# Performance work log

Measured on AMD Instinct MI355X. Metric: run time of the kernel, lower is better.

Reference implementation:

```python
import jax, jax.numpy as jnp
import numpy as np

N = 50000
E = 800000
IN_DIM = 256
HID = 64
HEADS0 = 4
HEADS1 = 1
NUM_CLASSES = 64
NEG_SLOPE = 0.2


def setup_inputs() -> dict:
    key = jax.random.key(0)
    ks = jax.random.split(key, 9)
    x = jax.random.normal(ks[0], (N, IN_DIM), dtype=jnp.float32)
    src0 = jax.random.randint(ks[1], (E,), 0, N, dtype=jnp.int32)
    dst0 = jax.random.randint(ks[2], (E,), 0, N, dtype=jnp.int32)
    src1 = jax.random.randint(ks[3], (E,), 0, N, dtype=jnp.int32)
    dst1 = jax.random.randint(ks[4], (E,), 0, N, dtype=jnp.int32)
    # layer 0: fc (share_weights -> single W), attn vector per head
    W0 = jax.random.normal(ks[5], (IN_DIM, HEADS0 * HID), dtype=jnp.float32) * (1.0 / np.sqrt(IN_DIM))
    attn0 = jax.random.normal(ks[6], (HEADS0, HID), dtype=jnp.float32) * (1.0 / np.sqrt(HID))
    # layer 1 (final): input dim = HID*HEADS0, out = NUM_CLASSES per head
    W1 = jax.random.normal(ks[7], (HID * HEADS0, HEADS1 * NUM_CLASSES), dtype=jnp.float32) * (1.0 / np.sqrt(HID * HEADS0))
    attn1 = jax.random.normal(ks[8], (HEADS1, NUM_CLASSES), dtype=jnp.float32) * (1.0 / np.sqrt(NUM_CLASSES))
    return {"x": x, "W0": W0, "attn0": attn0, "W1": W1, "attn1": attn1,
            "src0": src0, "dst0": dst0, "src1": src1, "dst1": dst1}


def gatv2_conv(h, W, attn, src, dst, n_nodes):
    """DGL GATv2Conv with share_weights=True, bias=False, residual=False.
    h: [N, Fin], W: [Fin, H*D], attn: [H, D]. Returns [N, H, D]."""
    H, D = attn.shape
    feat = (h @ W).reshape(n_nodes, H, D)          # [N, H, D]
    fs = feat[src]                                  # [E, H, D] gather src
    fd = feat[dst]                                  # [E, H, D] gather dst
    # e_ij = a^T LeakyReLU(W h_i + W h_j)
    e = jnp.einsum('ehd,hd->eh', jax.nn.leaky_relu(fs + fd, NEG_SLOPE), attn)  # [E, H]
    # edge softmax over incoming edges of each dst node (stable)
    m = jax.ops.segment_max(e, dst, num_segments=n_nodes)    # [N, H]
    ex = jnp.exp(e - m[dst])                                  # [E, H]
    s = jax.ops.segment_sum(ex, dst, num_segments=n_nodes)   # [N, H]
    alpha = ex / s[dst]                                       # [E, H]
    out = jax.ops.segment_sum(alpha[:, :, None] * fs, dst, num_segments=n_nodes)  # [N, H, D]
    return out


def reference(x, W0, attn0, W1, attn1, src0, dst0, src1, dst1):
    h = gatv2_conv(x, W0, attn0, src0, dst0, N)      # [N, 4, 64]
    h = jax.nn.elu(h)                                 # layer activation
    h = h.reshape(N, HEADS0 * HID)                    # flatten(1)
    h = gatv2_conv(h, W1, attn1, src1, dst1, N)       # [N, 1, 64], no activation
    logits = h.mean(axis=1)                           # mean over heads -> [N, 64]
    return logits
```

## Files before the change

kernel.cpp:

```cpp
#include <hip/hip_runtime.h>

#define N_NODES 50000
#define E_EDGES 800000
#define NEG_SLOPE 0.2f
#define NSL 8
#define SLN (NSL * N_NODES)
#define NB1 196
#define ROWS_PAD 50048
#define GB0 782
#define EB 3125
#define NBE0 12500
#define CAP 16

typedef __attribute__((ext_vector_type(8))) _Float16 f16x8;
typedef __attribute__((ext_vector_type(4))) float f32x4;
typedef __attribute__((ext_vector_type(4))) _Float16 half4v;
typedef __attribute__((ext_vector_type(2))) _Float16 half2v;

union H4 { half4v h4; half2v h2[2]; unsigned u[2]; };

__device__ __forceinline__ void gload_lds16(const void* g, void* l) {
    __builtin_amdgcn_global_load_lds((__attribute__((address_space(1))) void*)g,
                                     (__attribute__((address_space(3))) void*)l, 16, 0, 0);
}

#define LOG2E 1.4426950408889634f

__device__ __forceinline__ float score4(half4v g, half4v fd, const H4& A6, const H4& A4) {
    H4 Z; Z.h4 = g + fd;
    H4 B; B.u[0] = Z.u[0] & 0x7FFF7FFFu; B.u[1] = Z.u[1] & 0x7FFF7FFFu;
    float p = __builtin_amdgcn_fdot2(Z.h2[0], A6.h2[0], 0.0f, false);
    p = __builtin_amdgcn_fdot2(Z.h2[1], A6.h2[1], p, false);
    p = __builtin_amdgcn_fdot2(B.h2[0], A4.h2[0], p, false);
    p = __builtin_amdgcn_fdot2(B.h2[1], A4.h2[1], p, false);
    return p;
}

__device__ __forceinline__ void wimg_one(const float* W, _Float16* img, int Nc, int i) {
    int col = i >> 5, chunk = i & 31;
    int CT = Nc >> 4;
    int kb = chunk >> 2, ct = col >> 4;
    int li = (col & 15) + (chunk & 3) * 16;
    size_t base = ((size_t)kb * CT + ct) * 512 + li * 8;
    half4v v0, v1;
#pragma unroll
    for (int e = 0; e < 4; ++e) v0[e] = (_Float16)W[(size_t)(chunk * 8 + e) * Nc + col];
#pragma unroll
    for (int e = 0; e < 4; ++e) v1[e] = (_Float16)W[(size_t)(chunk * 8 + 4 + e) * Nc + col];
    *(half4v*)&img[base]     = v0;
    *(half4v*)&img[base + 4] = v1;
}


__global__ void k_init(const float* __restrict__ W0, const float* __restrict__ W1,
                       _Float16* __restrict__ img0, _Float16* __restrict__ img1,
                       int* __restrict__ cnt_s) {
    int gtid = blockIdx.x * 256 + threadIdx.x;
    if (gtid < 2 * SLN / 4) ((int4*)cnt_s)[gtid] = make_int4(0, 0, 0, 0);
    if (gtid < 256 * 32) wimg_one(W0, img0, 256, gtid);
    else if (gtid < 256 * 32 + 64 * 32) wimg_one(W1, img1, 64, gtid - 256 * 32);
}


__global__ __launch_bounds__(256, 4) void k_gemm0_scat(const float* __restrict__ X,
                                                       const _Float16* __restrict__ Bimg,
                                                       _Float16* __restrict__ C, int M,
                                                       const int* __restrict__ src0,
                                                       const int* __restrict__ dst0,
                                                       const int* __restrict__ src1,
                                                       const int* __restrict__ dst1,
                                                       int* __restrict__ cnt_s,
                                                       unsigned short* __restrict__ buck) {
    constexpr int CT = 16;
    __shared__ __align__(16) _Float16 AsF[4 * 512];
    __shared__ __align__(16) _Float16 Bs[CT * 512];

    if (blockIdx.x >= GB0) {
        int hb = blockIdx.x - GB0;
        int layer = (hb >= EB) ? 1 : 0;
        int bi = hb - layer * EB;
        int slice = bi & (NSL - 1);
        int i = bi * 256 + threadIdx.x;
        int s = (layer == 0) ? src0[i] : src1[i];
        int d = (layer == 0) ? dst0[i] : dst1[i];
        size_t sn = (size_t)layer * SLN + slice * N_NODES + d;
        int pos = atomicAdd(&cnt_s[sn], 1);
        if (pos < CAP) buck[(sn << 4) + pos] = (unsigned short)s;
        return;
    }

    const int t = threadIdx.x;
    const int w = t >> 6;
    const int lane = t & 63;
    const int r16 = lane & 15;
    const int kg = lane >> 4;
    const int bm = blockIdx.x * 64;
    const int arow = bm + w * 16 + r16;
    const bool rv = (arow < M);
    const float* xsrc = X + (size_t)arow * 256 + kg * 8;

    f32x4 acc[CT];
#pragma unroll
    for (int j = 0; j < CT; ++j) acc[j] = (f32x4){0.f, 0.f, 0.f, 0.f};

    for (int kb = 0; kb < 8; ++kb) {
        float4 v0 = make_float4(0.f, 0.f, 0.f, 0.f);
        float4 v1 = make_float4(0.f, 0.f, 0.f, 0.f);
        if (rv) {
            v0 = *(const float4*)(xsrc + kb * 32);
            v1 = *(const float4*)(xsrc + kb * 32 + 4);
        }
        f16x8 af;
        af[0] = (_Float16)v0.x; af[1] = (_Float16)v0.y;
        af[2] = (_Float16)v0.z; af[3] = (_Float16)v0.w;
        af[4] = (_Float16)v1.x; af[5] = (_Float16)v1.y;
        af[6] = (_Float16)v1.z; af[7] = (_Float16)v1.w;
        *(f16x8*)&AsF[t * 8] = af;
#pragma unroll
        for (int p = 0; p < CT / 4; ++p)
            gload_lds16(Bimg + kb * CT * 512 + p * 2048 + t * 8, &Bs[p * 2048 + w * 512]);
        __syncthreads();

        const f16x8 aF = *(const f16x8*)&AsF[t * 8];
#pragma unroll
        for (int ct = 0; ct < CT; ++ct) {
            const f16x8 b = *(const f16x8*)&Bs[ct * 512 + lane * 8];
            acc[ct] = __builtin_amdgcn_mfma_f32_16x16x32_f16(aF, b, acc[ct], 0, 0, 0);
        }
        __syncthreads();
    }

#pragma unroll
    for (int r = 0; r < 4; ++r) {
        int row = bm + w * 16 + kg * 4 + r;
        if (row < M) {
#pragma unroll
            for (int ct = 0; ct < CT; ++ct)
                C[(size_t)row * 256 + ct * 16 + r16] = (_Float16)acc[ct][r];
        }
    }
}


__global__ void k_scanA(const int* __restrict__ cnt_s, int* __restrict__ rowptr,
                        int* __restrict__ bsum1) {
    const int layer = blockIdx.y;
    __shared__ int lds[256];
    int t = threadIdx.x;
    int i = blockIdx.x * 256 + t;
    int v = 0;
    if (i < N_NODES) {
        const int* d = cnt_s + layer * SLN + i;
#pragma unroll
        for (int s = 0; s < NSL; ++s) v += d[s * N_NODES];
    }
    lds[t] = v;
    __syncthreads();
    for (int off = 1; off < 256; off <<= 1) {
        int u = (t >= off) ? lds[t - off] : 0;
        __syncthreads();
        lds[t] += u;
        __syncthreads();
    }
    if (i < N_NODES) rowptr[layer * (N_NODES + 1) + i + 1] = lds[t];
    if (t == 255) bsum1[layer * 256 + blockIdx.x] = lds[255];
}

__global__ void k_scanB(const int* __restrict__ bsum1, int* __restrict__ boff1) {
    const int layer = blockIdx.x;
    __shared__ int lds[256];
    int t = threadIdx.x;
    int v = (t < NB1) ? bsum1[layer * 256 + t] : 0;
    lds[t] = v;
    __syncthreads();
    for (int off = 1; off < 256; off <<= 1) {
        int u = (t >= off) ? lds[t - off] : 0;
        __syncthreads();
        lds[t] += u;
        __syncthreads();
    }
    if (t < NB1) boff1[layer * 256 + t] = lds[t] - v;
}

__global__ void k_scanC(const int* __restrict__ boff1, int* __restrict__ rowptr) {
    const int layer = blockIdx.y;
    int i = blockIdx.x * 256 + threadIdx.x;
    if (i >= N_NODES) return;
    int* rp = rowptr + layer * (N_NODES + 1);
    rp[i + 1] += boff1[layer * 256 + (i >> 8)];
    if (i == 0) rp[0] = 0;
}


__device__ __forceinline__ void regroup_node(const int* __restrict__ cnt_s,
                                             const int* __restrict__ rowptr,
                                             const unsigned short* __restrict__ buck,
                                             int* __restrict__ csr,
                                             int layer, int node, int lane, int sh) {
    const int base = layer * SLN;
    int dg = 0;
    if (lane < NSL) dg = cnt_s[base + lane * N_NODES + node];
    int excl = 0, total = 0;
#pragma unroll
    for (int ss = 0; ss < NSL; ++ss) {
        int v = __shfl(dg, ss);
        if (ss < (lane & 7)) excl += v;
        total += v;
    }
    const int base_out = rowptr[layer * (N_NODES + 1) + node];
    int* cdst = csr + (size_t)layer * E_EDGES;
    for (int r0 = 0; r0 < total; r0 += 64) {
        int r = r0 + lane;
        bool active = (r < total);
        int rr = active ? r : 0;
        int s = 0;
#pragma unroll
        for (int ss = 1; ss < NSL; ++ss) {
            int e = __shfl(excl, ss);
            if (rr >= e) s = ss;
        }
        int eS = __shfl(excl, s);
        if (active) {
            int val = buck[(((size_t)base + s * N_NODES + node) << 4) + (r - eS)];
            cdst[base_out + r] = val << sh;
        }
    }
}


__global__ __launch_bounds__(256) void k_regroup0(const int* __restrict__ cnt_s,
                                                  const int* __restrict__ rowptr,
                                                  const unsigned short* __restrict__ buck,
                                                  int* __restrict__ csr) {
    const int lane = threadIdx.x & 63;
    const int node = blockIdx.x * 4 + (threadIdx.x >> 6);
    if (node >= N_NODES) return;
    regroup_node(cnt_s, rowptr, buck, csr, 0, node, lane, 9);
}


__global__ __launch_bounds__(256) void gat_edge0(const _Float16* __restrict__ feat,
                                                 const float* __restrict__ attn,
                                                 const int* __restrict__ rowptr,
                                                 const int* __restrict__ csr,
                                                 _Float16* __restrict__ h0img) {
    const int lane = threadIdx.x & 63;
    const int node = blockIdx.x * 4 + (threadIdx.x >> 6);
    if (node >= N_NODES) return;
    const int dbase = ((lane >> 4) << 6) + (lane & 15) * 4;
    const float4 a = *(const float4*)&attn[dbase];
    H4 A6, A4;
    A6.h4 = (half4v){(_Float16)(0.6f * LOG2E * a.x), (_Float16)(0.6f * LOG2E * a.y),
                     (_Float16)(0.6f * LOG2E * a.z), (_Float16)(0.6f * LOG2E * a.w)};
    A4.h4 = (half4v){(_Float16)(0.4f * LOG2E * a.x), (_Float16)(0.4f * LOG2E * a.y),
                     (_Float16)(0.4f * LOG2E * a.z), (_Float16)(0.4f * LOG2E * a.w)};
    const char* fbase = (const char*)feat + dbase * 2;
    const half4v fd4 = *(const half4v*)(fbase + ((size_t)node << 9));
    const int beg = rowptr[node], end = rowptr[node + 1];
    float s = 0.f, ax = 0.f, ay = 0.f, az = 0.f, aw = 0.f;
    int j = beg;
    for (; j + 7 < end; j += 8) {
        half4v g[8];
        float p[8];
#pragma unroll
        for (int i = 0; i < 8; ++i) g[i] = *(const half4v*)(fbase + csr[j + i]);
#pragma unroll
        for (int i = 0; i < 8; ++i) p[i] = score4(g[i], fd4, A6, A4);
#pragma unroll
        for (int r = 1; r <= 8; r <<= 1)
#pragma unroll
            for (int i = 0; i < 8; ++i) p[i] += __shfl_xor(p[i], r);
        float e[8];
#pragma unroll
        for (int i = 0; i < 8; ++i) e[i] = __builtin_amdgcn_exp2f(p[i]);
#pragma unroll
        for (int i = 0; i < 8; ++i) {
            s  += e[i];
            ax += e[i] * (float)g[i][0];
            ay += e[i] * (float)g[i][1];
            az += e[i] * (float)g[i][2];
            aw += e[i] * (float)g[i][3];
        }
    }
    if (j + 3 < end) {
        half4v g[4];
        float p[4];
#pragma unroll
        for (int i = 0; i < 4; ++i) g[i] = *(const half4v*)(fbase + csr[j + i]);
#pragma unroll
        for (int i = 0; i < 4; ++i) p[i] = score4(g[i], fd4, A6, A4);
#pragma unroll
        for (int r = 1; r <= 8; r <<= 1)
#pragma unroll
            for (int i = 0; i < 4; ++i) p[i] += __shfl_xor(p[i], r);
#pragma unroll
        for (int i = 0; i < 4; ++i) {
            float e = __builtin_amdgcn_exp2f(p[i]);
            s  += e;
            ax += e * (float)g[i][0];
            ay += e * (float)g[i][1];
            az += e * (float)g[i][2];
            aw += e * (float)g[i][3];
        }
        j += 4;
    }
    for (; j < end; ++j) {
        half4v g0 = *(const half4v*)(fbase + csr[j]);
        float p0 = score4(g0, fd4, A6, A4);
        p0 += __shfl_xor(p0, 1);
        p0 += __shfl_xor(p0, 2);
        p0 += __shfl_xor(p0, 4);
        p0 += __shfl_xor(p0, 8);
        float e0 = __builtin_amdgcn_exp2f(p0);
        s  += e0;
        ax += e0 * (float)g0[0];
        ay += e0 * (float)g0[1];
        az += e0 * (float)g0[2];
        aw += e0 * (float)g0[3];
    }
    float inv = (end > beg) ? (1.0f / s) : 0.f;
    half4v o;
    float v;
    v = ax * inv; o[0] = (_Float16)((v > 0.f) ? v : (__expf(v) - 1.f));
    v = ay * inv; o[1] = (_Float16)((v > 0.f) ? v : (__expf(v) - 1.f));
    v = az * inv; o[2] = (_Float16)((v > 0.f) ? v : (__expf(v) - 1.f));
    v = aw * inv; o[3] = (_Float16)((v > 0.f) ? v : (__expf(v) - 1.f));
    const int rtg = node >> 4;
    const int kb = dbase >> 5;
    const int li = (node & 15) + ((dbase >> 3) & 3) * 16;
    const size_t idx = ((size_t)rtg * 8 + kb) * 512 + li * 8 + (dbase & 7);
    *(half4v*)&h0img[idx] = o;
}


__global__ __launch_bounds__(256, 4) void k_gemm1_regroup1(const _Float16* __restrict__ Aimg,
                                                           const _Float16* __restrict__ Bimg,
                                                           _Float16* __restrict__ C, int M,
                                                           const int* __restrict__ cnt_s,
                                                           const int* __restrict__ rowptr,
                                                           const unsigned short* __restrict__ buck,
                                                           int* __restrict__ csr) {
    constexpr int CT = 4;
    __shared__ __align__(16) _Float16 AsF[4 * 512];
    __shared__ __align__(16) _Float16 Bs[CT * 512];

    if (blockIdx.x >= GB0) {
        const int lane = threadIdx.x & 63;
        const int node = (blockIdx.x - GB0) * 4 + (threadIdx.x >> 6);
        if (node >= N_NODES) return;
        regroup_node(cnt_s, rowptr, buck, csr, 1, node, lane, 7);
        return;
    }

    const int t = threadIdx.x;
    const int w = t >> 6;
    const int lane = t & 63;
    const int r16 = lane & 15;
    const int kg = lane >> 4;
    const int bm = blockIdx.x * 64;

    f32x4 acc[CT];
#pragma unroll
    for (int j = 0; j < CT; ++j) acc[j] = (f32x4){0.f, 0.f, 0.f, 0.f};

    const size_t abase = ((size_t)(blockIdx.x * 4 + w)) * 8 * 512;

    for (int kb = 0; kb < 8; ++kb) {
        gload_lds16(Aimg + abase + kb * 512 + lane * 8, &AsF[w * 512]);
        gload_lds16(Bimg + kb * CT * 512 + t * 8, &Bs[w * 512]);
        __syncthreads();

        const f16x8 aF = *(const f16x8*)&AsF[w * 512 + lane * 8];
#pragma unroll
        for (int ct = 0; ct < CT; ++ct) {
            const f16x8 b = *(const f16x8*)&Bs[ct * 512 + lane * 8];
            acc[ct] = __builtin_amdgcn_mfma_f32_16x16x32_f16(aF, b, acc[ct], 0, 0, 0);
        }
        __syncthreads();
    }

#pragma unroll
    for (int r = 0; r < 4; ++r) {
        int row = bm + w * 16 + kg * 4 + r;
        if (row < M) {
#pragma unroll
            for (int ct = 0; ct < CT; ++ct)
                C[(size_t)row * 64 + ct * 16 + r16] = (_Float16)acc[ct][r];
        }
    }
}


__global__ __launch_bounds__(256) void gat_edge1(const _Float16* __restrict__ feat,
                                                 const float* __restrict__ attn,
                                                 const int* __restrict__ rowptr,
                                                 const int* __restrict__ csr,
                                                 float* __restrict__ out) {
    const int lane = threadIdx.x & 63;
    const int node = blockIdx.x * 4 + (threadIdx.x >> 6);
    if (node >= N_NODES) return;
    const int g = lane >> 4;
    const int d0 = (lane & 15) * 4;
    const float4 a = *(const float4*)&attn[d0];
    H4 A6, A4;
    A6.h4 = (half4v){(_Float16)(0.6f * LOG2E * a.x), (_Float16)(0.6f * LOG2E * a.y),
                     (_Float16)(0.6f * LOG2E * a.z), (_Float16)(0.6f * LOG2E * a.w)};
    A4.h4 = (half4v){(_Float16)(0.4f * LOG2E * a.x), (_Float16)(0.4f * LOG2E * a.y),
                     (_Float16)(0.4f * LOG2E * a.z), (_Float16)(0.4f * LOG2E * a.w)};
    const char* fbase = (const char*)feat + d0 * 2;
    const half4v fd4 = *(const half4v*)(fbase + ((size_t)node << 7));
    const int beg = rowptr[node], end = rowptr[node + 1];
    float s = 0.f, ax = 0.f, ay = 0.f, az = 0.f, aw = 0.f;
    int j = beg + g;
    for (; j + 4 < end; j += 8) {
        half4v g0 = *(const half4v*)(fbase + csr[j]);
        half4v g1 = *(const half4v*)(fbase + csr[j + 4]);
        float p0 = score4(g0, fd4, A6, A4);
        float p1 = score4(g1, fd4, A6, A4);
        p0 += __shfl_xor(p0, 1); p1 += __shfl_xor(p1, 1);
        p0 += __shfl_xor(p0, 2); p1 += __shfl_xor(p1, 2);
        p0 += __shfl_xor(p0, 4); p1 += __shfl_xor(p1, 4);
        p0 += __shfl_xor(p0, 8); p1 += __shfl_xor(p1, 8);
        float e0 = __builtin_amdgcn_exp2f(p0);
        float e1 = __builtin_amdgcn_exp2f(p1);
        s  += e0 + e1;
        ax += e0 * (float)g0[0] + e1 * (float)g1[0];
        ay += e0 * (float)g0[1] + e1 * (float)g1[1];
        az += e0 * (float)g0[2] + e1 * (float)g1[2];
        aw += e0 * (float)g0[3] + e1 * (float)g1[3];
    }
    if (j < end) {
        half4v g0 = *(const half4v*)(fbase + csr[j]);
        float p = score4(g0, fd4, A6, A4);
        p += __shfl_xor(p, 1);
        p += __shfl_xor(p, 2);
        p += __shfl_xor(p, 4);
        p += __shfl_xor(p, 8);
        float e = __builtin_amdgcn_exp2f(p);
        s  += e;
        ax += e * (float)g0[0];
        ay += e * (float)g0[1];
        az += e * (float)g0[2];
        aw += e * (float)g0[3];
    }
#pragma unroll
    for (int off = 16; off <= 32; off <<= 1) {
        s  += __shfl_xor(s, off);
        ax += __shfl_xor(ax, off);
        ay += __shfl_xor(ay, off);
        az += __shfl_xor(az, off);
        aw += __shfl_xor(aw, off);
    }
    if (g == 0) {
        float inv = (end > beg) ? (1.0f / s) : 0.f;
        float4 o = make_float4(ax * inv, ay * inv, az * inv, aw * inv);
        *(float4*)&out[(size_t)node * 64 + d0] = o;
    }
}


extern "C" void kernel_launch(void* const* d_in, const int* in_sizes, int n_in,
                              void* d_out, int out_size, void* d_ws, size_t ws_size,
                              hipStream_t stream) {
    const float* x     = (const float*)d_in[0];
    const float* W0    = (const float*)d_in[1];
    const float* attn0 = (const float*)d_in[2];
    const float* W1    = (const float*)d_in[3];
    const float* attn1 = (const float*)d_in[4];
    const int*   src0  = (const int*)d_in[5];
    const int*   dst0  = (const int*)d_in[6];
    const int*   src1  = (const int*)d_in[7];
    const int*   dst1  = (const int*)d_in[8];
    float* out = (float*)d_out;

    _Float16* h0img  = (_Float16*)d_ws;
    _Float16* feat0h = h0img + (size_t)ROWS_PAD * 256;
    _Float16* W0img  = feat0h + (size_t)N_NODES * 256;
    _Float16* W1img  = W0img + 256 * 256;
    _Float16* feat1h = feat0h;

    int* cnt_s  = (int*)(W1img + 64 * 256);
    int* rowptr = cnt_s + 2 * SLN;
    int* bsum1  = rowptr + 2 * (N_NODES + 1);
    int* boff1  = bsum1 + 512;
    int* csr    = boff1 + 512;
    unsigned short* buck = (unsigned short*)(csr + 2 * E_EDGES);

    k_init<<<GB0, 256, 0, stream>>>(W0, W1, W0img, W1img, cnt_s);

    k_gemm0_scat<<<GB0 + 2 * EB, 256, 0, stream>>>(x, W0img, feat0h, N_NODES,
                                                   src0, dst0, src1, dst1, cnt_s, buck);

    k_scanA<<<dim3(NB1, 2), 256, 0, stream>>>(cnt_s, rowptr, bsum1);
    k_scanB<<<2,            256, 0, stream>>>(bsum1, boff1);
    k_scanC<<<dim3(NB1, 2), 256, 0, stream>>>(boff1, rowptr);

    k_regroup0<<<NBE0, 256, 0, stream>>>(cnt_s, rowptr, buck, csr);

    gat_edge0<<<NBE0, 256, 0, stream>>>(feat0h, attn0, rowptr, csr, h0img);

    k_gemm1_regroup1<<<GB0 + NBE0, 256, 0, stream>>>(h0img, W1img, feat1h, N_NODES,
                                                     cnt_s, rowptr, buck, csr);

    gat_edge1<<<NBE0, 256, 0, stream>>>(feat1h, attn1, rowptr + (N_NODES + 1),
                                        csr + E_EDGES, out);
}
```

Measured before the change: 239.7 us.

## Drop CSR build; read edge buckets directly in edge-softmax kernels

Removes the three prefix-scan kernels and both regroup passes that turned per-slice buckets into a CSR array. The edge kernels now compute per-node slice prefixes with warp shuffles and gather neighbor offsets straight from the bucket array. Count zeroing moves to a memset, and the weight-image build is merged into the scatter kernel, which now runs separately from GEMM0. This cuts several launches and a full CSR write and read, but loses the overlap of the scatter with GEMM0. It also caps in-degree per slice at CAP, so edges beyond 16 per slice are silently dropped.

```diff
diff --git a/kernel.cpp b/kernel.cpp
--- a/kernel.cpp
+++ b/kernel.cpp
@@ -5,12 +5,12 @@
 #define NEG_SLOPE 0.2f
 #define NSL 8
 #define SLN (NSL * N_NODES)
-#define NB1 196
 #define ROWS_PAD 50048
 #define GB0 782
 #define EB 3125
 #define NBE0 12500
 #define CAP 16
+#define WIB 40
 
 typedef __attribute__((ext_vector_type(8))) _Float16 f16x8;
 typedef __attribute__((ext_vector_type(4))) float f32x4;
@@ -52,33 +52,14 @@
 }
 
 
-__global__ void k_init(const float* __restrict__ W0, const float* __restrict__ W1,
-                       _Float16* __restrict__ img0, _Float16* __restrict__ img1,
-                       int* __restrict__ cnt_s) {
-    int gtid = blockIdx.x * 256 + threadIdx.x;
-    if (gtid < 2 * SLN / 4) ((int4*)cnt_s)[gtid] = make_int4(0, 0, 0, 0);
-    if (gtid < 256 * 32) wimg_one(W0, img0, 256, gtid);
-    else if (gtid < 256 * 32 + 64 * 32) wimg_one(W1, img1, 64, gtid - 256 * 32);
-}
-
-
-__global__ __launch_bounds__(256, 4) void k_gemm0_scat(const float* __restrict__ X,
-                                                       const _Float16* __restrict__ Bimg,
-                                                       _Float16* __restrict__ C, int M,
-                                                       const int* __restrict__ src0,
-                                                       const int* __restrict__ dst0,
-                                                       const int* __restrict__ src1,
-                                                       const int* __restrict__ dst1,
-                                                       int* __restrict__ cnt_s,
-                                                       unsigned short* __restrict__ buck) {
-    constexpr int CT = 16;
-    __shared__ __align__(16) _Float16 AsF[4 * 512];
-    __shared__ __align__(16) _Float16 Bs[CT * 512];
-
-    if (blockIdx.x >= GB0) {
-        int hb = blockIdx.x - GB0;
-        int layer = (hb >= EB) ? 1 : 0;
-        int bi = hb - layer * EB;
+__global__ void k_scat_wimg(const int* __restrict__ src0, const int* __restrict__ dst0,
+                            const int* __restrict__ src1, const int* __restrict__ dst1,
+                            int* __restrict__ cnt_s, unsigned short* __restrict__ buck,
+                            const float* __restrict__ W0, const float* __restrict__ W1,
+                            _Float16* __restrict__ img0, _Float16* __restrict__ img1) {
+    if (blockIdx.x < 2 * EB) {
+        int layer = (blockIdx.x >= EB) ? 1 : 0;
+        int bi = blockIdx.x - layer * EB;
         int slice = bi & (NSL - 1);
         int i = bi * 256 + threadIdx.x;
         int s = (layer == 0) ? src0[i] : src1[i];
@@ -88,6 +69,18 @@
         if (pos < CAP) buck[(sn << 4) + pos] = (unsigned short)s;
         return;
     }
+    int gtid = (blockIdx.x - 2 * EB) * 256 + threadIdx.x;
+    if (gtid < 256 * 32) wimg_one(W0, img0, 256, gtid);
+    else if (gtid < 256 * 32 + 64 * 32) wimg_one(W1, img1, 64, gtid - 256 * 32);
+}
+
+
+__global__ __launch_bounds__(256, 4) void mfma_gemm0(const float* __restrict__ X,
+                                                     const _Float16* __restrict__ Bimg,
+                                                     _Float16* __restrict__ C, int M) {
+    constexpr int CT = 16;
+    __shared__ __align__(16) _Float16 AsF[4 * 512];
+    __shared__ __align__(16) _Float16 Bs[CT * 512];
 
     const int t = threadIdx.x;
     const int w = t >> 6;
@@ -142,107 +135,45 @@
 }
 
 
-__global__ void k_scanA(const int* __restrict__ cnt_s, int* __restrict__ rowptr,
-                        int* __restrict__ bsum1) {
-    const int layer = blockIdx.y;
-    __shared__ int lds[256];
-    int t = threadIdx.x;
-    int i = blockIdx.x * 256 + t;
-    int v = 0;
-    if (i < N_NODES) {
-        const int* d = cnt_s + layer * SLN + i;
-#pragma unroll
-        for (int s = 0; s < NSL; ++s) v += d[s * N_NODES];
-    }
-    lds[t] = v;
-    __syncthreads();
-    for (int off = 1; off < 256; off <<= 1) {
-        int u = (t >= off) ? lds[t - off] : 0;
-        __syncthreads();
-        lds[t] += u;
-        __syncthreads();
-    }
-    if (i < N_NODES) rowptr[layer * (N_NODES + 1) + i + 1] = lds[t];
-    if (t == 255) bsum1[layer * 256 + blockIdx.x] = lds[255];
-}
-
-__global__ void k_scanB(const int* __restrict__ bsum1, int* __restrict__ boff1) {
-    const int layer = blockIdx.x;
-    __shared__ int lds[256];
-    int t = threadIdx.x;
-    int v = (t < NB1) ? bsum1[layer * 256 + t] : 0;
-    lds[t] = v;
-    __syncthreads();
-    for (int off = 1; off < 256; off <<= 1) {
-        int u = (t >= off) ? lds[t - off] : 0;
-        __syncthreads();
-        lds[t] += u;
-        __syncthreads();
-    }
-    if (t < NB1) boff1[layer * 256 + t] = lds[t] - v;
-}
-
-__global__ void k_scanC(const int* __restrict__ boff1, int* __restrict__ rowptr) {
-    const int layer = blockIdx.y;
-    int i = blockIdx.x * 256 + threadIdx.x;
-    if (i >= N_NODES) return;
-    int* rp = rowptr + layer * (N_NODES + 1);
-    rp[i + 1] += boff1[layer * 256 + (i >> 8)];
-    if (i == 0) rp[0] = 0;
-}
-
-
-__device__ __forceinline__ void regroup_node(const int* __restrict__ cnt_s,
-                                             const int* __restrict__ rowptr,
-                                             const unsigned short* __restrict__ buck,
-                                             int* __restrict__ csr,
-                                             int layer, int node, int lane, int sh) {
-    const int base = layer * SLN;
-    int dg = 0;
-    if (lane < NSL) dg = cnt_s[base + lane * N_NODES + node];
-    int excl = 0, total = 0;
+__device__ __forceinline__ int bucket_prefix(const int* __restrict__ cnt_s,
+                                             int base, int node, int lane, int& excl) {
+    int c = 0;
+    if (lane < NSL) {
+        c = cnt_s[base + lane * N_NODES + node];
+        c = (c > CAP) ? CAP : c;
+    }
+    excl = 0;
+    int total = 0;
 #pragma unroll
     for (int ss = 0; ss < NSL; ++ss) {
-        int v = __shfl(dg, ss);
+        int v = __shfl(c, ss);
         if (ss < (lane & 7)) excl += v;
         total += v;
     }
-    const int base_out = rowptr[layer * (N_NODES + 1) + node];
-    int* cdst = csr + (size_t)layer * E_EDGES;
-    for (int r0 = 0; r0 < total; r0 += 64) {
-        int r = r0 + lane;
-        bool active = (r < total);
-        int rr = active ? r : 0;
-        int s = 0;
-#pragma unroll
-        for (int ss = 1; ss < NSL; ++ss) {
-            int e = __shfl(excl, ss);
-            if (rr >= e) s = ss;
-        }
-        int eS = __shfl(excl, s);
-        if (active) {
-            int val = buck[(((size_t)base + s * N_NODES + node) << 4) + (r - eS)];
-            cdst[base_out + r] = val << sh;
-        }
-    }
-}
-
-
-__global__ __launch_bounds__(256) void k_regroup0(const int* __restrict__ cnt_s,
-                                                  const int* __restrict__ rowptr,
-                                                  const unsigned short* __restrict__ buck,
-                                                  int* __restrict__ csr) {
-    const int lane = threadIdx.x & 63;
-    const int node = blockIdx.x * 4 + (threadIdx.x >> 6);
-    if (node >= N_NODES) return;
-    regroup_node(cnt_s, rowptr, buck, csr, 0, node, lane, 9);
+    return total;
+}
+
+__device__ __forceinline__ int bucket_offset(const unsigned short* __restrict__ buck,
+                                             int base, int node, int excl, int rr,
+                                             int total, int sh) {
+    int sl = 0;
+#pragma unroll
+    for (int ss = 1; ss < NSL; ++ss) {
+        int e = __shfl(excl, ss);
+        if (rr >= e) sl = ss;
+    }
+    int eS = __shfl(excl, sl);
+    int v = 0;
+    if (rr < total)
+        v = buck[(((size_t)base + sl * N_NODES + node) << 4) + (rr - eS)];
+    return v << sh;
 }
 
 
 __global__ __launch_bounds__(256) void gat_edge0(const _Float16* __restrict__ feat,
                                                  const float* __restrict__ attn,
-                                                 const int* __restrict__ rowptr,
-                                                 const int* __restrict__ csr,
+                                                 const int* __restrict__ cnt_s,
+                                                 const unsigned short* __restrict__ buck,
                                                  _Float16* __restrict__ h0img) {
     const int lane = threadIdx.x & 63;
     const int node = blockIdx.x * 4 + (threadIdx.x >> 6);
@@ -256,69 +187,76 @@
                      (_Float16)(0.4f * LOG2E * a.z), (_Float16)(0.4f * LOG2E * a.w)};
     const char* fbase = (const char*)feat + dbase * 2;
     const half4v fd4 = *(const half4v*)(fbase + ((size_t)node << 9));
-    const int beg = rowptr[node], end = rowptr[node + 1];
+
+    int excl;
+    const int total = bucket_prefix(cnt_s, 0, node, lane, excl);
+
     float s = 0.f, ax = 0.f, ay = 0.f, az = 0.f, aw = 0.f;
-    int j = beg;
-    for (; j + 7 < end; j += 8) {
-        half4v g[8];
-        float p[8];
-#pragma unroll
-        for (int i = 0; i < 8; ++i) g[i] = *(const half4v*)(fbase + csr[j + i]);
-#pragma unroll
-        for (int i = 0; i < 8; ++i) p[i] = score4(g[i], fd4, A6, A4);
-#pragma unroll
-        for (int r = 1; r <= 8; r <<= 1)
-#pragma unroll
-            for (int i = 0; i < 8; ++i) p[i] += __shfl_xor(p[i], r);
-        float e[8];
-#pragma unroll
-        for (int i = 0; i < 8; ++i) e[i] = __builtin_amdgcn_exp2f(p[i]);
-#pragma unroll
-        for (int i = 0; i < 8; ++i) {
-            s  += e[i];
-            ax += e[i] * (float)g[i][0];
-            ay += e[i] * (float)g[i][1];
-            az += e[i] * (float)g[i][2];
-            aw += e[i] * (float)g[i][3];
-        }
-    }
-    if (j + 3 < end) {
-        half4v g[4];
-        float p[4];
-#pragma unroll
-        for (int i = 0; i < 4; ++i) g[i] = *(const half4v*)(fbase + csr[j + i]);
-#pragma unroll
-        for (int i = 0; i < 4; ++i) p[i] = score4(g[i], fd4, A6, A4);
-#pragma unroll
-        for (int r = 1; r <= 8; r <<= 1)
-#pragma unroll
-            for (int i = 0; i < 4; ++i) p[i] += __shfl_xor(p[i], r);
-#pragma unroll
-        for (int i = 0; i < 4; ++i) {
-            float e = __builtin_amdgcn_exp2f(p[i]);
-            s  += e;
-            ax += e * (float)g[i][0];
-            ay += e * (float)g[i][1];
-            az += e * (float)g[i][2];
-            aw += e * (float)g[i][3];
-        }
-        j += 4;
-    }
-    for (; j < end; ++j) {
-        half4v g0 = *(const half4v*)(fbase + csr[j]);
-        float p0 = score4(g0, fd4, A6, A4);
-        p0 += __shfl_xor(p0, 1);
-        p0 += __shfl_xor(p0, 2);
-        p0 += __shfl_xor(p0, 4);
-        p0 += __shfl_xor(p0, 8);
-        float e0 = __builtin_amdgcn_exp2f(p0);
-        s  += e0;
-        ax += e0 * (float)g0[0];
-        ay += e0 * (float)g0[1];
-        az += e0 * (float)g0[2];
-        aw += e0 * (float)g0[3];
-    }
-    float inv = (end > beg) ? (1.0f / s) : 0.f;
+    for (int b = 0; b < total; b += 64) {
+        const int my_ofs = bucket_offset(buck, 0, node, excl, b + lane, total, 9);
+        const int ch = min(total - b, 64);
+        int i = 0;
+        for (; i + 7 < ch; i += 8) {
+            half4v g[8];
+            float p[8];
+#pragma unroll
+            for (int k = 0; k < 8; ++k) g[k] = *(const half4v*)(fbase + __shfl(my_ofs, i + k));
+#pragma unroll
+            for (int k = 0; k < 8; ++k) p[k] = score4(g[k], fd4, A6, A4);
+#pragma unroll
+            for (int r = 1; r <= 8; r <<= 1)
+#pragma unroll
+                for (int k = 0; k < 8; ++k) p[k] += __shfl_xor(p[k], r);
+            float e[8];
+#pragma unroll
+            for (int k = 0; k < 8; ++k) e[k] = __builtin_amdgcn_exp2f(p[k]);
+#pragma unroll
+            for (int k = 0; k < 8; ++k) {
+                s  += e[k];
+                ax += e[k] * (float)g[k][0];
+                ay += e[k] * (float)g[k][1];
+                az += e[k] * (float)g[k][2];
+                aw += e[k] * (float)g[k][3];
+            }
+        }
+        if (i + 3 < ch) {
+            half4v g[4];
+            float p[4];
+#pragma unroll
+            for (int k = 0; k < 4; ++k) g[k] = *(const half4v*)(fbase + __shfl(my_ofs, i + k));
+#pragma unroll
+            for (int k = 0; k < 4; ++k) p[k] = score4(g[k], fd4, A6, A4);
+#pragma unroll
+            for (int r = 1; r <= 8; r <<= 1)
+#pragma unroll
+                for (int k = 0; k < 4; ++k) p[k] += __shfl_xor(p[k], r);
+#pragma unroll
+            for (int k = 0; k < 4; ++k) {
+                float e = __builtin_amdgcn_exp2f(p[k]);
+                s  += e;
+                ax += e * (float)g[k][0];
+                ay += e * (float)g[k][1];
+                az += e * (float)g[k][2];
+                aw += e * (float)g[k][3];
+            }
+            i += 4;
+        }
+        for (; i < ch; ++i) {
+            half4v g0 = *(const half4v*)(fbase + __shfl(my_ofs, i));
+            float p0 = score4(g0, fd4, A6, A4);
+            p0 += __shfl_xor(p0, 1);
+            p0 += __shfl_xor(p0, 2);
+            p0 += __shfl_xor(p0, 4);
+            p0 += __shfl_xor(p0, 8);
+            float e0 = __builtin_amdgcn_exp2f(p0);
+            s  += e0;
+            ax += e0 * (float)g0[0];
+            ay += e0 * (float)g0[1];
+            az += e0 * (float)g0[2];
+            aw += e0 * (float)g0[3];
+        }
+    }
+    float inv = (total > 0) ? (1.0f / s) : 0.f;
     half4v o;
     float v;
     v = ax * inv; o[0] = (_Float16)((v > 0.f) ? v : (__expf(v) - 1.f));
@@ -333,24 +271,12 @@
 }
 
 
-__global__ __launch_bounds__(256, 4) void k_gemm1_regroup1(const _Float16* __restrict__ Aimg,
-                                                           const _Float16* __restrict__ Bimg,
-                                                           _Float16* __restrict__ C, int M,
-                                                           const int* __restrict__ cnt_s,
-                                                           const int* __restrict__ rowptr,
-                                                           const unsigned short* __restrict__ buck,
-                                                           int* __restrict__ csr) {
+__global__ __launch_bounds__(256, 4) void mfma_gemm1(const _Float16* __restrict__ Aimg,
+                                                     const _Float16* __restrict__ Bimg,
+                                                     _Float16* __restrict__ C, int M) {
     constexpr int CT = 4;
     __shared__ __align__(16) _Float16 AsF[4 * 512];
     __shared__ __align__(16) _Float16 Bs[CT * 512];
-
-    if (blockIdx.x >= GB0) {
-        const int lane = threadIdx.x & 63;
-        const int node = (blockIdx.x - GB0) * 4 + (threadIdx.x >> 6);
-        if (node >= N_NODES) return;
-        regroup_node(cnt_s, rowptr, buck, csr, 1, node, lane, 7);
-        return;
-    }
 
     const int t = threadIdx.x;
     const int w = t >> 6;
@@ -393,8 +319,8 @@
 
 __global__ __launch_bounds__(256) void gat_edge1(const _Float16* __restrict__ feat,
                                                  const float* __restrict__ attn,
-                                                 const int* __restrict__ rowptr,
-                                                 const int* __restrict__ csr,
+                                                 const int* __restrict__ cnt_s,
+                                                 const unsigned short* __restrict__ buck,
                                                  float* __restrict__ out) {
     const int lane = threadIdx.x & 63;
     const int node = blockIdx.x * 4 + (threadIdx.x >> 6);
@@ -409,39 +335,38 @@
                      (_Float16)(0.4f * LOG2E * a.z), (_Float16)(0.4f * LOG2E * a.w)};
     const char* fbase = (const char*)feat + d0 * 2;
     const half4v fd4 = *(const half4v*)(fbase + ((size_t)node << 7));
-    const int beg = rowptr[node], end = rowptr[node + 1];
+
+    int excl;
+    const int total = bucket_prefix(cnt_s, SLN, node, lane, excl);
+
     float s = 0.f, ax = 0.f, ay = 0.f, az = 0.f, aw = 0.f;
-    int j = beg + g;
-    for (; j + 4 < end; j += 8) {
-        half4v g0 = *(const half4v*)(fbase + csr[j]);
-        half4v g1 = *(const half4v*)(fbase + csr[j + 4]);
-        float p0 = score4(g0, fd4, A6, A4);
-        float p1 = score4(g1, fd4, A6, A4);
-        p0 += __shfl_xor(p0, 1); p1 += __shfl_xor(p1, 1);
-        p0 += __shfl_xor(p0, 2); p1 += __shfl_xor(p1, 2);
-        p0 += __shfl_xor(p0, 4); p1 += __shfl_xor(p1, 4);
-        p0 += __shfl_xor(p0, 8); p1 += __shfl_xor(p1, 8);
-        float e0 = __builtin_amdgcn_exp2f(p0);
-        float e1 = __builtin_amdgcn_exp2f(p1);
-        s  += e0 + e1;
-        ax += e0 * (float)g0[0] + e1 * (float)g1[0];
-        ay += e0 * (float)g0[1] + e1 * (float)g1[1];
-        az += e0 * (float)g0[2] + e1 * (float)g1[2];
-        aw += e0 * (float)g0[3] + e1 * (float)g1[3];
-    }
-    if (j < end) {
-        half4v g0 = *(const half4v*)(fbase + csr[j]);
-        float p = score4(g0, fd4, A6, A4);
-        p += __shfl_xor(p, 1);
-        p += __shfl_xor(p, 2);
-        p += __shfl_xor(p, 4);
-        p += __shfl_xor(p, 8);
-        float e = __builtin_amdgcn_exp2f(p);
-        s  += e;
-        ax += e * (float)g0[0];
-        ay += e * (float)g0[1];
-        az += e * (float)g0[2];
-        aw += e * (float)g0[3];
+    for (int b = 0; b < total; b += 64) {
+        const int my_ofs = bucket_offset(buck, SLN, node, excl, b + lane, total, 7);
+        const int ch = min(total - b, 64);
+        const int rounds = (ch + 3) >> 2;
+        for (int m = 0; m < rounds; m += 2) {
+            const int e0 = 4 * m + g;
+            const int e1 = e0 + 4;
+            const int o0 = __shfl(my_ofs, e0 & 63);
+            const int o1 = __shfl(my_ofs, e1 & 63);
+            const bool v0 = (e0 < ch);
+            const bool v1 = (e1 < ch);
+            half4v g0 = *(const half4v*)(fbase + o0);
+            half4v g1 = *(const half4v*)(fbase + o1);
+            float p0 = score4(g0, fd4, A6, A4);
+            float p1 = score4(g1, fd4, A6, A4);
+            p0 += __shfl_xor(p0, 1); p1 += __shfl_xor(p1, 1);
+            p0 += __shfl_xor(p0, 2); p1 += __shfl_xor(p1, 2);
+            p0 += __shfl_xor(p0, 4); p1 += __shfl_xor(p1, 4);
+            p0 += __shfl_xor(p0, 8); p1 += __shfl_xor(p1, 8);
+            float e0f = v0 ? __builtin_amdgcn_exp2f(p0) : 0.f;
+            float e1f = v1 ? __builtin_amdgcn_exp2f(p1) : 0.f;
+            s  += e0f + e1f;
+            ax += e0f * (float)g0[0] + e1f * (float)g1[0];
+            ay += e0f * (float)g0[1] + e1f * (float)g1[1];
+            az += e0f * (float)g0[2] + e1f * (float)g1[2];
+            aw += e0f * (float)g0[3] + e1f * (float)g1[3];
+        }
     }
 #pragma unroll
     for (int off = 16; off <= 32; off <<= 1) {
@@ -452,7 +377,7 @@
         aw += __shfl_xor(aw, off);
     }
     if (g == 0) {
-        float inv = (end > beg) ? (1.0f / s) : 0.f;
+        float inv = (total > 0) ? (1.0f / s) : 0.f;
         float4 o = make_float4(ax * inv, ay * inv, az * inv, aw * inv);
         *(float4*)&out[(size_t)node * 64 + d0] = o;
     }
@@ -479,29 +404,19 @@
     _Float16* W1img  = W0img + 256 * 256;
     _Float16* feat1h = feat0h;
 
-    int* cnt_s  = (int*)(W1img + 64 * 256);
-    int* rowptr = cnt_s + 2 * SLN;
-    int* bsum1  = rowptr + 2 * (N_NODES + 1);
-    int* boff1  = bsum1 + 512;
-    int* csr    = boff1 + 512;
-    unsigned short* buck = (unsigned short*)(csr + 2 * E_EDGES);
-
-    k_init<<<GB0, 256, 0, stream>>>(W0, W1, W0img, W1img, cnt_s);
-
-    k_gemm0_scat<<<GB0 + 2 * EB, 256, 0, stream>>>(x, W0img, feat0h, N_NODES,
-                                                   src0, dst0, src1, dst1, cnt_s, buck);
-
-    k_scanA<<<dim3(NB1, 2), 256, 0, stream>>>(cnt_s, rowptr, bsum1);
-    k_scanB<<<2,            256, 0, stream>>>(bsum1, boff1);
-    k_scanC<<<dim3(NB1, 2), 256, 0, stream>>>(boff1, rowptr);
-
-    k_regroup0<<<NBE0, 256, 0, stream>>>(cnt_s, rowptr, buck, csr);
-
-    gat_edge0<<<NBE0, 256, 0, stream>>>(feat0h, attn0, rowptr, csr, h0img);
-
-    k_gemm1_regroup1<<<GB0 + NBE0, 256, 0, stream>>>(h0img, W1img, feat1h, N_NODES,
-                                                     cnt_s, rowptr, buck, csr);
-
-    gat_edge1<<<NBE0, 256, 0, stream>>>(feat1h, attn1, rowptr + (N_NODES + 1),
-                                        csr + E_EDGES, out);
-}
+    int* cnt_s = (int*)(W1img + 64 * 256);
+    unsigned short* buck = (unsigned short*)(cnt_s + 2 * SLN);
+
+    hipMemsetAsync(cnt_s, 0, 2 * SLN * sizeof(int), stream);
+
+    k_scat_wimg<<<2 * EB + WIB, 256, 0, stream>>>(src0, dst0, src1, dst1, cnt_s, buck,
+                                                  W0, W1, W0img, W1img);
+
+    mfma_gemm0<<<GB0, 256, 0, stream>>>(x, W0img, feat0h, N_NODES);
+
+    gat_edge0<<<NBE0, 256, 0, stream>>>(feat0h, attn0, cnt_s, buck, h0img);
+
+    mfma_gemm1<<<GB0, 256, 0, stream>>>(h0img, W1img, feat1h, N_NODES);
+
+    gat_edge1<<<NBE0, 256, 0, stream>>>(feat1h, attn1, cnt_s, buck, out);
+}
```

Measured after the change: 246.5 us. +2.8%, slower.
